# Optimization experiments

Measured on AMD Instinct MI355X. Metric: run time of the kernel, lower is better.

The kernel has to match this reference:

```python
import jax, jax.numpy as jnp
import numpy as np

B, H, S, D = 4, 16, 2048, 64

def setup_inputs() -> dict:
    key = jax.random.key(0)
    kq, kk, kv = jax.random.split(key, 3)
    q = jax.random.normal(kq, (B, H, S, D), dtype=jnp.float32)
    k = jax.random.normal(kk, (B, H, S, D), dtype=jnp.float32)
    v = jax.random.normal(kv, (B, H, S, D), dtype=jnp.float32)
    # causal mask: True where attention is DISALLOWED (masked_fill semantics)
    row = jnp.arange(S)[:, None]
    col = jnp.arange(S)[None, :]
    attn_mask = (col > row)[None, None, :, :]  # [1,1,S,S] bool
    return {"q": q, "k": k, "v": v, "attn_mask": attn_mask}

def reference(q, k, v, attn_mask):
    scale = 1.0 / jnp.sqrt(jnp.float32(q.shape[-1]))
    # [B,H,S,S] scores
    scores = jnp.einsum("bhqd,bhkd->bhqk", q, k) * scale
    scores = jnp.where(attn_mask, -jnp.inf, scores)
    attn = jax.nn.softmax(scores, axis=-1)
    # dropout p=0 (eval) -> identity
    context = jnp.einsum("bhqk,bhkd->bhqd", attn, v)
    return context
```

## Files before the change

### kernel.cpp

```cpp
#include <hip/hip_runtime.h>

#define BB 4
#define HH 16
#define SS 2048
#define DD 64
#define NTILE (SS / 64)
#define BLOB_U16 8192

typedef __bf16 bf16x8 __attribute__((ext_vector_type(8)));
typedef __bf16 bf16x2 __attribute__((ext_vector_type(2)));
typedef float  f32x4  __attribute__((ext_vector_type(4)));
typedef unsigned short u16;
typedef unsigned int   u32;
typedef unsigned int   u32x2 __attribute__((ext_vector_type(2)));

__device__ __forceinline__ u16 f2bf(float f) {
    u32 u = __float_as_uint(f);
    u = (u + 0x7fffu + ((u >> 16) & 1u)) >> 16;
    return (u16)u;
}

__device__ __forceinline__ u32 pack2bf(float a, float b) {
#if __has_builtin(__builtin_amdgcn_cvt_pk_bf16_f32)
    bf16x2 t = __builtin_amdgcn_cvt_pk_bf16_f32(a, b);
    return __builtin_bit_cast(u32, t);
#else
    return (u32)f2bf(a) | ((u32)f2bf(b) << 16);
#endif
}

__device__ __forceinline__ u32x2 pl32(u32 a, u32 b) {
#if __has_builtin(__builtin_amdgcn_permlane32_swap)
    return __builtin_amdgcn_permlane32_swap(a, b, false, false);
#else
    asm("v_permlane32_swap_b32 %0, %1" : "+v"(a), "+v"(b));
    u32x2 r; r.x = a; r.y = b; return r;
#endif
}
__device__ __forceinline__ u32x2 pl16(u32 a, u32 b) {
#if __has_builtin(__builtin_amdgcn_permlane16_swap)
    return __builtin_amdgcn_permlane16_swap(a, b, false, false);
#else
    asm("v_permlane16_swap_b32 %0, %1" : "+v"(a), "+v"(b));
    u32x2 r; r.x = a; r.y = b; return r;
#endif
}

__device__ __forceinline__ void dma16(const void* g, const void* l) {
    __builtin_amdgcn_global_load_lds(
        (const __attribute__((address_space(1))) void*)g,
        (__attribute__((address_space(3))) void*)l, 16, 0, 0);
}

__global__ void prep(const float* __restrict__ k, const float* __restrict__ v,
                     u16* __restrict__ ws)
{
    __shared__ u16 tile[64 * 68];
    const int bh = blockIdx.y, ti = blockIdx.x, tid = threadIdx.x;
    const size_t ibase = (size_t)bh * SS * DD + (size_t)ti * 64 * DD;
    u16* blob = ws + (size_t)(bh * NTILE + ti) * BLOB_U16;

    {
        const float4* ks4 = (const float4*)(k + ibase) + tid * 4;
        union { u16 h[16]; uint4 u[2]; } ok;
        #pragma unroll
        for (int j = 0; j < 4; ++j) {
            float4 b = ks4[j];
            ok.h[j*4+0] = f2bf(b.x); ok.h[j*4+1] = f2bf(b.y);
            ok.h[j*4+2] = f2bf(b.z); ok.h[j*4+3] = f2bf(b.w);
        }
        const int r  = tid >> 2;
        const int c2 = (tid & 3) * 2;
        u16* kd = blob + r * 64;
        *(uint4*)(kd + ((c2    ) ^ (r & 7)) * 8) = ok.u[0];
        *(uint4*)(kd + ((c2 + 1) ^ (r & 7)) * 8) = ok.u[1];
    }
    {
        const int s4 = (tid >> 4) * 4;
        const int d4 = (tid & 15) * 4;
        float4 r0 = *(const float4*)(v + ibase + (size_t)(s4 + 0) * DD + d4);
        float4 r1 = *(const float4*)(v + ibase + (size_t)(s4 + 1) * DD + d4);
        float4 r2 = *(const float4*)(v + ibase + (size_t)(s4 + 2) * DD + d4);
        float4 r3 = *(const float4*)(v + ibase + (size_t)(s4 + 3) * DD + d4);
        const float c0[4] = {r0.x, r0.y, r0.z, r0.w};
        const float c1[4] = {r1.x, r1.y, r1.z, r1.w};
        const float c2[4] = {r2.x, r2.y, r2.z, r2.w};
        const float c3[4] = {r3.x, r3.y, r3.z, r3.w};
        #pragma unroll
        for (int i = 0; i < 4; ++i) {
            uint2 o;
            o.x = pack2bf(c0[i], c1[i]);
            o.y = pack2bf(c2[i], c3[i]);
            *(uint2*)(&tile[(d4 + i) * 68 + s4]) = o;
        }
    }
    __syncthreads();
    const int d  = tid >> 2;
    const int ch = tid & 3;
    uint4 o0 = *(const uint4*)(&tile[d * 68 + ch * 16]);
    uint4 o1 = *(const uint4*)(&tile[d * 68 + ch * 16 + 8]);
    u16* vd = blob + 4096 + d * 64;
    *(uint4*)(vd + ((ch * 2    ) ^ (d & 7)) * 8) = o0;
    *(uint4*)(vd + ((ch * 2 + 1) ^ (d & 7)) * 8) = o1;
}

__global__ __launch_bounds__(256, 4) void fa3(
    const float* __restrict__ q, const u16* __restrict__ ws,
    float* __restrict__ out)
{
    const int tid  = threadIdx.x;
    const int lane = tid & 63;
    const int w    = tid >> 6;
    const int quad = lane >> 4;
    const int m16  = lane & 15;
    const int bx   = blockIdx.x;
    const int rr   = bx >> 8;
    const int cc   = bx & 255;
    const int jj   = cc >> 6;
    const int bh   = cc & 63;
    const int qblk = (rr & 1) ? (12 - 4 * rr + jj) : (15 - 4 * rr - jj);
    const size_t base = (size_t)bh * SS * DD;
    const int qw0 = qblk * 128 + w * 32;

    __shared__ __align__(16) u16 KV[2 * BLOB_U16];

    const int swz   = (m16 & 7) << 4;
    const int offA0 = m16 * 128 + ((quad * 16) ^ swz);
    const int offA1 = m16 * 128 + ((quad * 16 + 64) ^ swz);

    const float qsc = 0.18033688011112042f;
    bf16x8 qf[2][2];
    #pragma unroll
    for (int qs = 0; qs < 2; ++qs)
        #pragma unroll
        for (int dc = 0; dc < 2; ++dc) {
            const float* qp = q + base + (size_t)(qw0 + qs * 16 + m16) * DD
                              + dc * 32 + quad * 8;
            float4 a = *(const float4*)(qp);
            float4 b = *(const float4*)(qp + 4);
            union { u32 u[4]; bf16x8 v; } t;
            t.u[0] = pack2bf(a.x * qsc, a.y * qsc);
            t.u[1] = pack2bf(a.z * qsc, a.w * qsc);
            t.u[2] = pack2bf(b.x * qsc, b.y * qsc);
            t.u[3] = pack2bf(b.z * qsc, b.w * qsc);
            qf[qs][dc] = t.v;
        }

    const f32x4 vzero = {0.f, 0.f, 0.f, 0.f};
    f32x4 acc[2][4];
    float lrow[2] = {0.f, 0.f};
    #pragma unroll
    for (int qs = 0; qs < 2; ++qs)
        #pragma unroll
        for (int dt = 0; dt < 4; ++dt) acc[qs][dt] = vzero;

    const int ntiles = qblk * 2 + 2;
    const char* gsrcT = (const char*)ws + (size_t)bh * NTILE * 16384
                        + (size_t)tid * 16;
    const int wbase = w * 512;

    {
        #pragma unroll
        for (int j = 0; j < 4; ++j)
            dma16(gsrcT + j * 4096, KV + wbase + j * 2048);
    }

    for (int t = 0; t < ntiles; ++t) {
        const int kv0 = t * 64;
        asm volatile("s_waitcnt vmcnt(0)" ::: "memory");
        __syncthreads();
        const char* Bb = (const char*)KV + (t & 1) * 16384;

        if (t + 1 < ntiles) {
            const char* g = gsrcT + (size_t)(t + 1) * 16384;
            const u16*  l = KV + ((t + 1) & 1) * BLOB_U16 + wbase;
            #pragma unroll
            for (int j = 0; j < 4; ++j)
                dma16(g + j * 4096, l + j * 2048);
        }

        if (kv0 <= qw0 + 31) {
            u32 pp[2][4][2];
            #pragma unroll
            for (int st = 0; st < 4; ++st) {
                const bf16x8 kf0 = *(const bf16x8*)(Bb + st * 2048 + offA0);
                const bf16x8 kf1 = *(const bf16x8*)(Bb + st * 2048 + offA1);
                #pragma unroll
                for (int qs = 0; qs < 2; ++qs) {
                    f32x4 s = __builtin_amdgcn_mfma_f32_16x16x32_bf16(
                        kf0, qf[qs][0], vzero, 0, 0, 0);
                    s = __builtin_amdgcn_mfma_f32_16x16x32_bf16(
                        kf1, qf[qs][1], s, 0, 0, 0);
                    const int q0 = qw0 + qs * 16;
                    if (kv0 + 63 > q0) {
                        const int qq = q0 + m16;
                        const int kb = kv0 + st * 16 + quad * 4;
                        #pragma unroll
                        for (int r = 0; r < 4; ++r)
                            if (kb + r > qq) s[r] = -1e30f;
                    }
                    const float p0 = __builtin_exp2f(s[0]);
                    const float p1 = __builtin_exp2f(s[1]);
                    const float p2 = __builtin_exp2f(s[2]);
                    const float p3 = __builtin_exp2f(s[3]);
                    lrow[qs] += (p0 + p2) + (p1 + p3);
                    pp[qs][st][0] = pack2bf(p0, p1);
                    pp[qs][st][1] = pack2bf(p2, p3);
                }
            }
            bf16x8 pfv[2][2];
            #pragma unroll
            for (int qs = 0; qs < 2; ++qs)
                #pragma unroll
                for (int kc = 0; kc < 2; ++kc) {
                    u32x2 t0 = pl32(pp[qs][2 * kc][0], pp[qs][2 * kc + 1][0]);
                    u32x2 r0 = pl16(t0.x, t0.y);
                    u32x2 t1 = pl32(pp[qs][2 * kc][1], pp[qs][2 * kc + 1][1]);
                    u32x2 r1 = pl16(t1.x, t1.y);
                    union { u32 u[4]; bf16x8 v; } pfu;
                    pfu.u[0] = r0.x; pfu.u[1] = r1.x;
                    pfu.u[2] = r0.y; pfu.u[3] = r1.y;
                    pfv[qs][kc] = pfu.v;
                }
            #pragma unroll
            for (int dt = 0; dt < 4; ++dt) {
                const bf16x8 vf0 = *(const bf16x8*)(Bb + 8192 + dt * 2048 + offA0);
                const bf16x8 vf1 = *(const bf16x8*)(Bb + 8192 + dt * 2048 + offA1);
                #pragma unroll
                for (int qs = 0; qs < 2; ++qs) {
                    acc[qs][dt] = __builtin_amdgcn_mfma_f32_16x16x32_bf16(
                        vf0, pfv[qs][0], acc[qs][dt], 0, 0, 0);
                    acc[qs][dt] = __builtin_amdgcn_mfma_f32_16x16x32_bf16(
                        vf1, pfv[qs][1], acc[qs][dt], 0, 0, 0);
                }
            }
        }
    }

    #pragma unroll
    for (int qs = 0; qs < 2; ++qs) {
        float l = lrow[qs];
        l += __shfl_xor(l, 16);
        l += __shfl_xor(l, 32);
        const float inv = 1.f / l;
        const int qq = qw0 + qs * 16 + m16;
        #pragma unroll
        for (int dt = 0; dt < 4; ++dt) {
            float4 o = make_float4(acc[qs][dt][0] * inv, acc[qs][dt][1] * inv,
                                   acc[qs][dt][2] * inv, acc[qs][dt][3] * inv);
            *(float4*)(out + base + (size_t)qq * DD + dt * 16 + quad * 4) = o;
        }
    }
}

extern "C" void kernel_launch(void* const* d_in, const int* in_sizes, int n_in,
                              void* d_out, int out_size, void* d_ws, size_t ws_size,
                              hipStream_t stream)
{
    const float* q = (const float*)d_in[0];
    const float* k = (const float*)d_in[1];
    const float* v = (const float*)d_in[2];
    float* out = (float*)d_out;

    u16* ws = (u16*)d_ws;

    prep<<<dim3(NTILE, BB * HH), dim3(256), 0, stream>>>(k, v, ws);
    fa3<<<dim3(16 * 64), dim3(256), 0, stream>>>(q, ws, out);
}
```

Baseline: 209.9 us.

## Pair complementary causal query blocks per workgroup and compute row sums via MFMA

```diff
diff --git a/kernel.cpp b/kernel.cpp
--- a/kernel.cpp
+++ b/kernel.cpp
@@ -104,7 +104,109 @@
     *(uint4*)(vd + ((ch * 2 + 1) ^ (d & 7)) * 8) = o1;
 }
 
-__global__ __launch_bounds__(256, 4) void fa3(
+template<bool DOU>
+__device__ __forceinline__ void fa_tile(
+    const char* __restrict__ Bb, const int kv0,
+    const bf16x8 (&qf)[2][2],
+    const int s0L, const int s0U,
+    const int m16, const int quad, const int offA0, const int offA1,
+    const bf16x8 ones,
+    f32x4 (&accL)[4], f32x4 (&accU)[4], f32x4 &laccL, f32x4 &laccU)
+{
+    const f32x4 vzero = {0.f, 0.f, 0.f, 0.f};
+    u32 ppL[4][2], ppU[4][2];
+    #pragma unroll
+    for (int st = 0; st < 4; ++st) {
+        const bf16x8 kf0 = *(const bf16x8*)(Bb + st * 2048 + offA0);
+        const bf16x8 kf1 = *(const bf16x8*)(Bb + st * 2048 + offA1);
+        {
+            f32x4 s = __builtin_amdgcn_mfma_f32_16x16x32_bf16(
+                kf0, qf[0][0], vzero, 0, 0, 0);
+            s = __builtin_amdgcn_mfma_f32_16x16x32_bf16(
+                kf1, qf[0][1], s, 0, 0, 0);
+            if (kv0 + 63 > s0L) {
+                const int qq = s0L + m16;
+                const int kb = kv0 + st * 16 + quad * 4;
+                #pragma unroll
+                for (int r = 0; r < 4; ++r)
+                    if (kb + r > qq) s[r] = -1e30f;
+            }
+            const float p0 = __builtin_exp2f(s[0]);
+            const float p1 = __builtin_exp2f(s[1]);
+            const float p2 = __builtin_exp2f(s[2]);
+            const float p3 = __builtin_exp2f(s[3]);
+            ppL[st][0] = pack2bf(p0, p1);
+            ppL[st][1] = pack2bf(p2, p3);
+        }
+        if (DOU) {
+            f32x4 s = __builtin_amdgcn_mfma_f32_16x16x32_bf16(
+                kf0, qf[1][0], vzero, 0, 0, 0);
+            s = __builtin_amdgcn_mfma_f32_16x16x32_bf16(
+                kf1, qf[1][1], s, 0, 0, 0);
+            if (kv0 + 63 > s0U) {
+                const int qq = s0U + m16;
+                const int kb = kv0 + st * 16 + quad * 4;
+                #pragma unroll
+                for (int r = 0; r < 4; ++r)
+                    if (kb + r > qq) s[r] = -1e30f;
+            }
+            const float p0 = __builtin_exp2f(s[0]);
+            const float p1 = __builtin_exp2f(s[1]);
+            const float p2 = __builtin_exp2f(s[2]);
+            const float p3 = __builtin_exp2f(s[3]);
+            ppU[st][0] = pack2bf(p0, p1);
+            ppU[st][1] = pack2bf(p2, p3);
+        }
+    }
+    bf16x8 pfL[2], pfU[2];
+    #pragma unroll
+    for (int kc = 0; kc < 2; ++kc) {
+        u32x2 t0 = pl32(ppL[2 * kc][0], ppL[2 * kc + 1][0]);
+        u32x2 r0 = pl16(t0.x, t0.y);
+        u32x2 t1 = pl32(ppL[2 * kc][1], ppL[2 * kc + 1][1]);
+        u32x2 r1 = pl16(t1.x, t1.y);
+        union { u32 u[4]; bf16x8 v; } pfu;
+        pfu.u[0] = r0.x; pfu.u[1] = r1.x;
+        pfu.u[2] = r0.y; pfu.u[3] = r1.y;
+        pfL[kc] = pfu.v;
+    }
+    if (DOU) {
+        #pragma unroll
+        for (int kc = 0; kc < 2; ++kc) {
+            u32x2 t0 = pl32(ppU[2 * kc][0], ppU[2 * kc + 1][0]);
+            u32x2 r0 = pl16(t0.x, t0.y);
+            u32x2 t1 = pl32(ppU[2 * kc][1], ppU[2 * kc + 1][1]);
+            u32x2 r1 = pl16(t1.x, t1.y);
+            union { u32 u[4]; bf16x8 v; } pfu;
+            pfu.u[0] = r0.x; pfu.u[1] = r1.x;
+            pfu.u[2] = r0.y; pfu.u[3] = r1.y;
+            pfU[kc] = pfu.v;
+        }
+    }
+    laccL = __builtin_amdgcn_mfma_f32_16x16x32_bf16(ones, pfL[0], laccL, 0, 0, 0);
+    laccL = __builtin_amdgcn_mfma_f32_16x16x32_bf16(ones, pfL[1], laccL, 0, 0, 0);
+    if (DOU) {
+        laccU = __builtin_amdgcn_mfma_f32_16x16x32_bf16(ones, pfU[0], laccU, 0, 0, 0);
+        laccU = __builtin_amdgcn_mfma_f32_16x16x32_bf16(ones, pfU[1], laccU, 0, 0, 0);
+    }
+    #pragma unroll
+    for (int dt = 0; dt < 4; ++dt) {
+        const bf16x8 vf0 = *(const bf16x8*)(Bb + 8192 + dt * 2048 + offA0);
+        const bf16x8 vf1 = *(const bf16x8*)(Bb + 8192 + dt * 2048 + offA1);
+        accL[dt] = __builtin_amdgcn_mfma_f32_16x16x32_bf16(
+            vf0, pfL[0], accL[dt], 0, 0, 0);
+        accL[dt] = __builtin_amdgcn_mfma_f32_16x16x32_bf16(
+            vf1, pfL[1], accL[dt], 0, 0, 0);
+        if (DOU) {
+            accU[dt] = __builtin_amdgcn_mfma_f32_16x16x32_bf16(
+                vf0, pfU[0], accU[dt], 0, 0, 0);
+            accU[dt] = __builtin_amdgcn_mfma_f32_16x16x32_bf16(
+                vf1, pfU[1], accU[dt], 0, 0, 0);
+        }
+    }
+}
+
+__global__ __launch_bounds__(512, 4) void fa3(
     const float* __restrict__ q, const u16* __restrict__ ws,
     float* __restrict__ out)
 {
@@ -115,12 +217,12 @@
     const int m16  = lane & 15;
     const int bx   = blockIdx.x;
     const int rr   = bx >> 8;
-    const int cc   = bx & 255;
-    const int jj   = cc >> 6;
-    const int bh   = cc & 63;
-    const int qblk = (rr & 1) ? (12 - 4 * rr + jj) : (15 - 4 * rr - jj);
+    const int jj   = (bx >> 6) & 3;
+    const int bh   = bx & 63;
+    const int a    = rr ? (7 - jj) : jj;
     const size_t base = (size_t)bh * SS * DD;
-    const int qw0 = qblk * 128 + w * 32;
+    const int s0U = a * 128 + w * 16;
+    const int s0L = (15 - a) * 128 + w * 16;
 
     __shared__ __align__(16) u16 KV[2 * BLOB_U16];
 
@@ -131,38 +233,41 @@
     const float qsc = 0.18033688011112042f;
     bf16x8 qf[2][2];
     #pragma unroll
-    for (int qs = 0; qs < 2; ++qs)
+    for (int sx = 0; sx < 2; ++sx) {
+        const int s0 = sx ? s0U : s0L;
         #pragma unroll
         for (int dc = 0; dc < 2; ++dc) {
-            const float* qp = q + base + (size_t)(qw0 + qs * 16 + m16) * DD
+            const float* qp = q + base + (size_t)(s0 + m16) * DD
                               + dc * 32 + quad * 8;
-            float4 a = *(const float4*)(qp);
-            float4 b = *(const float4*)(qp + 4);
+            float4 fa = *(const float4*)(qp);
+            float4 fb = *(const float4*)(qp + 4);
             union { u32 u[4]; bf16x8 v; } t;
-            t.u[0] = pack2bf(a.x * qsc, a.y * qsc);
-            t.u[1] = pack2bf(a.z * qsc, a.w * qsc);
-            t.u[2] = pack2bf(b.x * qsc, b.y * qsc);
-            t.u[3] = pack2bf(b.z * qsc, b.w * qsc);
-            qf[qs][dc] = t.v;
-        }
+            t.u[0] = pack2bf(fa.x * qsc, fa.y * qsc);
+            t.u[1] = pack2bf(fa.z * qsc, fa.w * qsc);
+            t.u[2] = pack2bf(fb.x * qsc, fb.y * qsc);
+            t.u[3] = pack2bf(fb.z * qsc, fb.w * qsc);
+            qf[sx][dc] = t.v;
+        }
+    }
 
     const f32x4 vzero = {0.f, 0.f, 0.f, 0.f};
-    f32x4 acc[2][4];
-    float lrow[2] = {0.f, 0.f};
-    #pragma unroll
-    for (int qs = 0; qs < 2; ++qs)
-        #pragma unroll
-        for (int dt = 0; dt < 4; ++dt) acc[qs][dt] = vzero;
-
-    const int ntiles = qblk * 2 + 2;
+    f32x4 accL[4], accU[4], laccL = vzero, laccU = vzero;
+    #pragma unroll
+    for (int dt = 0; dt < 4; ++dt) { accL[dt] = vzero; accU[dt] = vzero; }
+
+    union { u32 u[4]; bf16x8 v; } onesu;
+    onesu.u[0] = 0x3F803F80u; onesu.u[1] = 0x3F803F80u;
+    onesu.u[2] = 0x3F803F80u; onesu.u[3] = 0x3F803F80u;
+    const bf16x8 ones = onesu.v;
+
+    const int ntiles = 32 - 2 * a;
     const char* gsrcT = (const char*)ws + (size_t)bh * NTILE * 16384
                         + (size_t)tid * 16;
-    const int wbase = w * 512;
-
-    {
-        #pragma unroll
-        for (int j = 0; j < 4; ++j)
-            dma16(gsrcT + j * 4096, KV + wbase + j * 2048);
+
+    {
+        u16* l = KV + tid * 8;
+        dma16(gsrcT, l);
+        dma16(gsrcT + 8192, l + 4096);
     }
 
     for (int t = 0; t < ntiles; ++t) {
@@ -173,81 +278,40 @@
 
         if (t + 1 < ntiles) {
             const char* g = gsrcT + (size_t)(t + 1) * 16384;
-            const u16*  l = KV + ((t + 1) & 1) * BLOB_U16 + wbase;
-            #pragma unroll
-            for (int j = 0; j < 4; ++j)
-                dma16(g + j * 4096, l + j * 2048);
-        }
-
-        if (kv0 <= qw0 + 31) {
-            u32 pp[2][4][2];
-            #pragma unroll
-            for (int st = 0; st < 4; ++st) {
-                const bf16x8 kf0 = *(const bf16x8*)(Bb + st * 2048 + offA0);
-                const bf16x8 kf1 = *(const bf16x8*)(Bb + st * 2048 + offA1);
-                #pragma unroll
-                for (int qs = 0; qs < 2; ++qs) {
-                    f32x4 s = __builtin_amdgcn_mfma_f32_16x16x32_bf16(
-                        kf0, qf[qs][0], vzero, 0, 0, 0);
-                    s = __builtin_amdgcn_mfma_f32_16x16x32_bf16(
-                        kf1, qf[qs][1], s, 0, 0, 0);
-                    const int q0 = qw0 + qs * 16;
-                    if (kv0 + 63 > q0) {
-                        const int qq = q0 + m16;
-                        const int kb = kv0 + st * 16 + quad * 4;
-                        #pragma unroll
-                        for (int r = 0; r < 4; ++r)
-                            if (kb + r > qq) s[r] = -1e30f;
-                    }
-                    const float p0 = __builtin_exp2f(s[0]);
-                    const float p1 = __builtin_exp2f(s[1]);
-                    const float p2 = __builtin_exp2f(s[2]);
-                    const float p3 = __builtin_exp2f(s[3]);
-                    lrow[qs] += (p0 + p2) + (p1 + p3);
-                    pp[qs][st][0] = pack2bf(p0, p1);
-                    pp[qs][st][1] = pack2bf(p2, p3);
-                }
-            }
-            bf16x8 pfv[2][2];
-            #pragma unroll
-            for (int qs = 0; qs < 2; ++qs)
-                #pragma unroll
-                for (int kc = 0; kc < 2; ++kc) {
-                    u32x2 t0 = pl32(pp[qs][2 * kc][0], pp[qs][2 * kc + 1][0]);
-                    u32x2 r0 = pl16(t0.x, t0.y);
-                    u32x2 t1 = pl32(pp[qs][2 * kc][1], pp[qs][2 * kc + 1][1]);
-                    u32x2 r1 = pl16(t1.x, t1.y);
-                    union { u32 u[4]; bf16x8 v; } pfu;
-                    pfu.u[0] = r0.x; pfu.u[1] = r1.x;
-                    pfu.u[2] = r0.y; pfu.u[3] = r1.y;
-                    pfv[qs][kc] = pfu.v;
-                }
-            #pragma unroll
-            for (int dt = 0; dt < 4; ++dt) {
-                const bf16x8 vf0 = *(const bf16x8*)(Bb + 8192 + dt * 2048 + offA0);
-                const bf16x8 vf1 = *(const bf16x8*)(Bb + 8192 + dt * 2048 + offA1);
-                #pragma unroll
-                for (int qs = 0; qs < 2; ++qs) {
-                    acc[qs][dt] = __builtin_amdgcn_mfma_f32_16x16x32_bf16(
-                        vf0, pfv[qs][0], acc[qs][dt], 0, 0, 0);
-                    acc[qs][dt] = __builtin_amdgcn_mfma_f32_16x16x32_bf16(
-                        vf1, pfv[qs][1], acc[qs][dt], 0, 0, 0);
-                }
-            }
-        }
-    }
-
-    #pragma unroll
-    for (int qs = 0; qs < 2; ++qs) {
-        float l = lrow[qs];
-        l += __shfl_xor(l, 16);
-        l += __shfl_xor(l, 32);
-        const float inv = 1.f / l;
-        const int qq = qw0 + qs * 16 + m16;
+            u16* l = KV + ((t + 1) & 1) * BLOB_U16 + tid * 8;
+            dma16(g, l);
+            dma16(g + 8192, l + 4096);
+        }
+
+        const bool doL = (kv0 <= s0L + 15);
+        const bool doU = (kv0 <= s0U + 15);
+        if (doL) {
+            if (doU)
+                fa_tile<true >(Bb, kv0, qf, s0L, s0U, m16, quad, offA0, offA1,
+                               ones, accL, accU, laccL, laccU);
+            else
+                fa_tile<false>(Bb, kv0, qf, s0L, s0U, m16, quad, offA0, offA1,
+                               ones, accL, accU, laccL, laccU);
+        }
+    }
+
+    {
+        const float inv = 1.f / laccL[0];
+        const int qq = s0L + m16;
         #pragma unroll
         for (int dt = 0; dt < 4; ++dt) {
-            float4 o = make_float4(acc[qs][dt][0] * inv, acc[qs][dt][1] * inv,
-                                   acc[qs][dt][2] * inv, acc[qs][dt][3] * inv);
+            float4 o = make_float4(accL[dt][0] * inv, accL[dt][1] * inv,
+                                   accL[dt][2] * inv, accL[dt][3] * inv);
+            *(float4*)(out + base + (size_t)qq * DD + dt * 16 + quad * 4) = o;
+        }
+    }
+    {
+        const float inv = 1.f / laccU[0];
+        const int qq = s0U + m16;
+        #pragma unroll
+        for (int dt = 0; dt < 4; ++dt) {
+            float4 o = make_float4(accU[dt][0] * inv, accU[dt][1] * inv,
+                                   accU[dt][2] * inv, accU[dt][3] * inv);
             *(float4*)(out + base + (size_t)qq * DD + dt * 16 + quad * 4) = o;
         }
     }
@@ -265,5 +329,5 @@
     u16* ws = (u16*)d_ws;
 
     prep<<<dim3(NTILE, BB * HH), dim3(256), 0, stream>>>(k, v, ws);
-    fa3<<<dim3(16 * 64), dim3(256), 0, stream>>>(q, ws, out);
-}
+    fa3<<<dim3(8 * 64), dim3(512), 0, stream>>>(q, ws, out);
+}
```

Measured after the change: 210.4 us. Within noise of the previous version (+0.2%).
